# Kernel optimization log

Measured on AMD Instinct MI355X. Metric: run time of the kernel, lower is better.

Reference implementation:

```python
import jax, jax.numpy as jnp
import numpy as np

N, IN_DIM, HID, H1, NCLS, H2, E = 50000, 256, 32, 8, 16, 8, 800000


def gat_conv(x, edge_index, W, a_src, a_dst, b, H, C):
    """PyG-style GATConv, eval mode (attention dropout off), concat=True,
    negative_slope=0.2, add_self_loops=True."""
    n = x.shape[0]
    loop = jnp.arange(n)
    src = jnp.concatenate([edge_index[0], loop])  # [E+N]
    dst = jnp.concatenate([edge_index[1], loop])
    h = (x @ W).reshape(n, H, C)                  # [N,H,C]
    alpha_s = jnp.sum(h * a_src, axis=-1)         # [N,H]
    alpha_d = jnp.sum(h * a_dst, axis=-1)         # [N,H]
    e = jax.nn.leaky_relu(alpha_s[src] + alpha_d[dst], 0.2)  # [E+N,H]
    # segment softmax over incoming edges of each target node
    e_max = jax.ops.segment_max(e, dst, num_segments=n)      # [N,H] (self-loop guarantees nonempty)
    p = jnp.exp(e - e_max[dst])
    denom = jax.ops.segment_sum(p, dst, num_segments=n)
    alpha = p / (denom[dst] + 1e-16)              # [E+N,H]
    msg = h[src] * alpha[:, :, None]              # [E+N,H,C]
    out = jax.ops.segment_sum(msg, dst, num_segments=n)      # [N,H,C]
    return out.reshape(n, H * C) + b


def setup_inputs() -> dict:
    key = jax.random.key(0)
    ks = jax.random.split(key, 12)
    x = jax.random.normal(ks[0], (N, IN_DIM), dtype=jnp.float32)
    edge_index = jax.random.randint(ks[1], (2, E), 0, N, dtype=jnp.int64)
    s1 = 1.0 / np.sqrt(IN_DIM)
    s2 = 1.0 / np.sqrt(HID * H1)
    W1 = jax.random.normal(ks[2], (IN_DIM, H1 * HID), dtype=jnp.float32) * s1
    a_src1 = jax.random.normal(ks[3], (H1, HID), dtype=jnp.float32) * s1
    a_dst1 = jax.random.normal(ks[4], (H1, HID), dtype=jnp.float32) * s1
    b1 = jnp.zeros((H1 * HID,), dtype=jnp.float32)
    W2 = jax.random.normal(ks[5], (H1 * HID, H2 * NCLS), dtype=jnp.float32) * s2
    a_src2 = jax.random.normal(ks[6], (H2, NCLS), dtype=jnp.float32) * s2
    a_dst2 = jax.random.normal(ks[7], (H2, NCLS), dtype=jnp.float32) * s2
    b2 = jnp.zeros((H2 * NCLS,), dtype=jnp.float32)
    return {"x": x, "edge_index": edge_index, "W1": W1, "a_src1": a_src1,
            "a_dst1": a_dst1, "b1": b1, "W2": W2, "a_src2": a_src2,
            "a_dst2": a_dst2, "b2": b2}


def reference(x, edge_index, W1, a_src1, a_dst1, b1, W2, a_src2, a_dst2, b2):
    # eval mode: F.dropout is identity
    h = gat_conv(x, edge_index, W1, a_src1, a_dst1, b1, H1, HID)   # [N, H1*HID]
    h = jax.nn.elu(h)
    h = gat_conv(h, edge_index, W2, a_src2, a_dst2, b2, H2, NCLS)  # [N, H2*NCLS]
    return jax.nn.log_softmax(h, axis=1)
```

## Files before the change

### kernel.cpp

```cpp
#include <hip/hip_runtime.h>
#include <hip/hip_fp16.h>

#define NN 50000
#define NE 800000

typedef _Float16 half4v __attribute__((ext_vector_type(4)));
typedef _Float16 half8v __attribute__((ext_vector_type(8)));
typedef float f32x4 __attribute__((ext_vector_type(4)));

#define Q_SCALE 0.04724409448f
#define Q_INV   21.16666667f

static __device__ __forceinline__ float lrelu(float x) { return x > 0.f ? x : 0.2f * x; }

__global__ void detect_i64_kernel(const unsigned* __restrict__ ei, int* __restrict__ flag) {
  if (threadIdx.x == 0 && blockIdx.x == 0) {
    int is64 = 1;
    for (int i = 0; i < 64; ++i)
      if (ei[2 * i + 1] != 0u) { is64 = 0; break; }
    *flag = is64;
  }
}

static __device__ __forceinline__ int edge_at(const void* ei, int is64, long long idx) {
  if (is64) return (int)((const long long*)ei)[idx];
  return ((const int*)ei)[idx];
}

__global__ void count_kernel(const void* __restrict__ ei, const int* __restrict__ flag,
                             int* __restrict__ counts) {
  int e = blockIdx.x * blockDim.x + threadIdx.x;
  if (e >= NE) return;
  int is64 = *flag;
  int d = edge_at(ei, is64, (long long)NE + e);
  atomicAdd(&counts[d], 1);
}

static __device__ __forceinline__ int block_scan_inc(int v, int tid) {
  __shared__ int ws[4];
  const int lane = tid & 63, wv = tid >> 6;
  #pragma unroll
  for (int off = 1; off < 64; off <<= 1) {
    int t = __shfl_up(v, off);
    if (lane >= off) v += t;
  }
  if (lane == 63) ws[wv] = v;
  __syncthreads();
  int add = 0;
  #pragma unroll
  for (int j = 0; j < 4; ++j) if (j < wv) add += ws[j];
  return v + add;
}

__global__ void scan1_kernel(const int* __restrict__ counts, int* __restrict__ bsums) {
  __shared__ int ws[4];
  const int tid = threadIdx.x;
  const int lane = tid & 63, wv = tid >> 6;
  int i = blockIdx.x * 256 + tid;
  int v = (i < NN) ? counts[i] : 0;
  #pragma unroll
  for (int off = 1; off < 64; off <<= 1) v += __shfl_xor(v, off);
  if (lane == 0) ws[wv] = v;
  __syncthreads();
  if (tid == 0) bsums[blockIdx.x] = ws[0] + ws[1] + ws[2] + ws[3];
}

__global__ void scan2_kernel(int* __restrict__ bsums, int nb) {
  const int tid = threadIdx.x;
  int v = (tid < nb) ? bsums[tid] : 0;
  int inc = block_scan_inc(v, tid);
  if (tid < nb) bsums[tid] = inc - v;
}

__global__ void scan3_kernel(const int* __restrict__ counts, const int* __restrict__ bsums,
                             int* __restrict__ rs) {
  const int tid = threadIdx.x;
  int i = blockIdx.x * 256 + tid;
  int v = (i < NN) ? counts[i] : 0;
  int inc = block_scan_inc(v, tid);
  if (i < NN) rs[i + 1] = bsums[blockIdx.x] + inc;
  if (i == 0) rs[0] = 0;
}

__global__ void scatter_kernel(const void* __restrict__ ei, const int* __restrict__ flag,
                               const int* __restrict__ rs, int* __restrict__ cursor,
                               int* __restrict__ ssrc) {
  int e = blockIdx.x * blockDim.x + threadIdx.x;
  if (e >= NE) return;
  int is64 = *flag;
  int s = edge_at(ei, is64, e);
  int d = edge_at(ei, is64, (long long)NE + e);
  int p = atomicAdd(&cursor[d], 1);
  ssrc[rs[d] + p] = s;
}

__global__ void prep_kernel(const float* __restrict__ W1, const float* __restrict__ W2,
                            const float* __restrict__ aS1, const float* __restrict__ aD1,
                            const float* __restrict__ aS2, const float* __restrict__ aD2,
                            _Float16* __restrict__ W1p, _Float16* __restrict__ W2p,
                            _Float16* __restrict__ Wa1p, _Float16* __restrict__ Wa2p) {
  int i = blockIdx.x * blockDim.x + threadIdx.x;
  if (i < 65536) {
    int j = i & 7, l = (i >> 3) & 63, kst = (i >> 9) & 7, ct = i >> 12;
    int col = ct * 16 + (l & 15);
    int k = kst * 32 + ((l >> 4) << 3) + j;
    W1p[i] = (_Float16)W1[(size_t)k * 256 + col];
  } else if (i < 98304) {
    int n = i - 65536;
    int j = n & 7, l = (n >> 3) & 63, kst = (n >> 9) & 7, ct = n >> 12;
    int col = ct * 16 + (l & 15);
    int k = kst * 32 + ((l >> 4) << 3) + j;
    W2p[n] = (_Float16)W2[(size_t)k * 128 + col];
  } else if (i < 102400) {
    int n = i - 98304;
    int j = n & 7, l = (n >> 3) & 63, kst = n >> 9;
    int row = l & 15;
    int head = row & 7;
    const float* a = (row < 8) ? aS1 : aD1;
    int k = kst * 32 + ((l >> 4) << 3) + j;
    float s = 0.f;
    #pragma unroll 8
    for (int c = 0; c < 32; ++c)
      s += W1[(size_t)k * 256 + head * 32 + c] * a[head * 32 + c];
    Wa1p[n] = (_Float16)s;
  } else if (i < 106496) {
    int n = i - 102400;
    int j = n & 7, l = (n >> 3) & 63, kst = n >> 9;
    int row = l & 15;
    int head = row & 7;
    const float* a = (row < 8) ? aS2 : aD2;
    int k = kst * 32 + ((l >> 4) << 3) + j;
    float s = 0.f;
    #pragma unroll 8
    for (int c = 0; c < 16; ++c)
      s += W2[(size_t)k * 128 + head * 16 + c] * a[head * 16 + c];
    Wa2p[n] = (_Float16)s;
  }
}

template<int BN, int NCF, bool A_HALF, bool Q8OUT>
__global__ __launch_bounds__(512) void gemm_mfma(const void* __restrict__ Araw,
                                                 const _Float16* __restrict__ Bp,
                                                 const _Float16* __restrict__ Wap,
                                                 void* __restrict__ Cout,
                                                 float* __restrict__ alS,
                                                 float* __restrict__ alD, int M) {
  __shared__ __align__(16) _Float16 As[64][256 + 8];
  const int tid = threadIdx.x;
  const int bm0 = blockIdx.x * 64;
  if (A_HALF) {
    const _Float16* A = (const _Float16*)Araw;
    half8v tmp[4]; int rr[4], cc[4];
    #pragma unroll
    for (int t = 0; t < 4; ++t) {
      int idx = tid + t * 512;
      int r = idx >> 5, c8 = (idx & 31) << 3;
      int gr = bm0 + r;
      tmp[t] = (half8v){};
      if (gr < M) tmp[t] = *(const half8v*)&A[(size_t)gr * 256 + c8];
      rr[t] = r; cc[t] = c8;
    }
    #pragma unroll
    for (int t = 0; t < 4; ++t)
      *(half8v*)&As[rr[t]][cc[t]] = tmp[t];
  } else {
    const float* A = (const float*)Araw;
    #pragma unroll
    for (int g = 0; g < 2; ++g) {
      float4 tmp[4]; int rr[4], cc[4];
      #pragma unroll
      for (int t = 0; t < 4; ++t) {
        int idx = tid + (g * 4 + t) * 512;
        int r = idx >> 6, c4 = (idx & 63) << 2;
        int gr = bm0 + r;
        tmp[t] = make_float4(0.f, 0.f, 0.f, 0.f);
        if (gr < M) tmp[t] = *(const float4*)&A[(size_t)gr * 256 + c4];
        rr[t] = r; cc[t] = c4;
      }
      #pragma unroll
      for (int t = 0; t < 4; ++t) {
        half4v h = { (_Float16)tmp[t].x, (_Float16)tmp[t].y,
                     (_Float16)tmp[t].z, (_Float16)tmp[t].w };
        *(half4v*)&As[rr[t]][cc[t]] = h;
      }
    }
  }
  __syncthreads();
  const int lane = tid & 63, wv = tid >> 6;
  const int ncol0 = wv * (16 * NCF);
  const int lrow = lane & 15, lk8 = (lane >> 4) << 3;
  f32x4 acc[4][NCF];
  f32x4 acca[4];
  #pragma unroll
  for (int rf = 0; rf < 4; ++rf) {
    acca[rf] = (f32x4){0.f, 0.f, 0.f, 0.f};
    #pragma unroll
    for (int cf = 0; cf < NCF; ++cf) acc[rf][cf] = (f32x4){0.f, 0.f, 0.f, 0.f};
  }
  #pragma unroll
  for (int kst = 0; kst < 8; ++kst) {
    const int ks = kst * 32 + lk8;
    half8v af[4];
    #pragma unroll
    for (int rf = 0; rf < 4; ++rf)
      af[rf] = *(const half8v*)&As[16 * rf + lrow][ks];
    #pragma unroll
    for (int cf = 0; cf < NCF; ++cf) {
      half8v bf = *(const half8v*)&Bp[((size_t)((wv * NCF + cf) * 8 + kst) * 64 + lane) * 8];
      #pragma unroll
      for (int rf = 0; rf < 4; ++rf)
        acc[rf][cf] = __builtin_amdgcn_mfma_f32_16x16x32_f16(af[rf], bf, acc[rf][cf], 0, 0, 0);
    }
    if (wv == 0) {
      half8v bfa = *(const half8v*)&Wap[((size_t)kst * 64 + lane) * 8];
      #pragma unroll
      for (int rf = 0; rf < 4; ++rf)
        acca[rf] = __builtin_amdgcn_mfma_f32_16x16x32_f16(af[rf], bfa, acca[rf], 0, 0, 0);
    }
  }
  if (Q8OUT) {
    __syncthreads();
    constexpr int ROWB = BN + 16;
    char* Cs = (char*)&As[0][0];
    #pragma unroll
    for (int rf = 0; rf < 4; ++rf) {
      #pragma unroll
      for (int j = 0; j < 4; ++j) {
        int r = 16 * rf + 4 * ((lane >> 4) & 3) + j;
        #pragma unroll
        for (int cf = 0; cf < NCF; ++cf) {
          int col = ncol0 + 16 * cf + lrow;
          float v = acc[rf][cf][j];
          int q = __float2int_rn(fminf(fmaxf(v * Q_INV, -127.f), 127.f)) + 128;
          Cs[r * ROWB + col] = (char)q;
        }
      }
    }
    __syncthreads();
    unsigned char* C8 = (unsigned char*)Cout;
    for (int idx = tid; idx < 4 * BN; idx += 512) {
      int r = idx / (BN / 16), c16 = idx % (BN / 16);
      int grow = bm0 + r;
      if (grow < M)
        *(int4*)&C8[(size_t)grow * BN + 16 * c16] = *(const int4*)&Cs[r * ROWB + 16 * c16];
    }
  } else {
    __half* C = (__half*)Cout;
    #pragma unroll
    for (int rf = 0; rf < 4; ++rf) {
      #pragma unroll
      for (int j = 0; j < 4; ++j) {
        int row = bm0 + 16 * rf + 4 * ((lane >> 4) & 3) + j;
        if (row < M) {
          #pragma unroll
          for (int cf = 0; cf < NCF; ++cf) {
            int col = ncol0 + 16 * cf + lrow;
            C[(size_t)row * BN + col] = __float2half(acc[rf][cf][j]);
          }
        }
      }
    }
  }
  if (wv == 0) {
    #pragma unroll
    for (int rf = 0; rf < 4; ++rf) {
      #pragma unroll
      for (int j = 0; j < 4; ++j) {
        int row = bm0 + 16 * rf + 4 * ((lane >> 4) & 3) + j;
        if (row < M) {
          float v = acca[rf][j];
          if (lrow < 8) alS[row * 8 + lrow] = v;
          else          alD[row * 8 + (lrow - 8)] = v;
        }
      }
    }
  }
}

#define ACCQ(w, p) do { \
    ax0 += (p) * (float)((w) & 255u); \
    ax1 += (p) * (float)(((w) >> 8) & 255u); \
    ax2 += (p) * (float)(((w) >> 16) & 255u); \
    ax3 += (p) * (float)((w) >> 24); \
  } while (0)

__global__ __launch_bounds__(256) void agg1_kernel(const unsigned char* __restrict__ h1q,
    const float* __restrict__ as, const float* __restrict__ ad,
    const int* __restrict__ rs, const int* __restrict__ ssrc,
    const float* __restrict__ bias, __half* __restrict__ out) {
  const int wid = (blockIdx.x * blockDim.x + threadIdx.x) >> 6;
  const int lane = threadIdx.x & 63;
  if (wid >= NN) return;
  const int node = wid;
  const int beg = rs[node], end = rs[node + 1];
  const int deg = end - beg;
  const int hd = lane >> 3;
  const float advh = ad[node * 8 + hd];
  const unsigned* hw = (const unsigned*)h1q;
  float denom = 0.f;
  float ax0 = 0.f, ax1 = 0.f, ax2 = 0.f, ax3 = 0.f;
  {
    float p = __expf(lrelu(as[node * 8 + hd] + advh));
    unsigned w = hw[(size_t)node * 64 + lane];
    ACCQ(w, p);
    denom = p;
  }
  const int gb = lane & 56;
  for (int base = 0; base < deg; base += 64) {
    const int cnt = min(deg - base, 64);
    int sv = (lane < cnt) ? ssrc[beg + base + lane] : 0;
    int j = 0;
    for (; j + 8 <= cnt; j += 8) {
      int s0 = __builtin_amdgcn_readlane(sv, j + 0);
      int s1 = __builtin_amdgcn_readlane(sv, j + 1);
      int s2 = __builtin_amdgcn_readlane(sv, j + 2);
      int s3 = __builtin_amdgcn_readlane(sv, j + 3);
      int s4 = __builtin_amdgcn_readlane(sv, j + 4);
      int s5 = __builtin_amdgcn_readlane(sv, j + 5);
      int s6 = __builtin_amdgcn_readlane(sv, j + 6);
      int s7 = __builtin_amdgcn_readlane(sv, j + 7);
      unsigned w0 = hw[(size_t)s0 * 64 + lane];
      unsigned w1 = hw[(size_t)s1 * 64 + lane];
      unsigned w2 = hw[(size_t)s2 * 64 + lane];
      unsigned w3 = hw[(size_t)s3 * 64 + lane];
      unsigned w4 = hw[(size_t)s4 * 64 + lane];
      unsigned w5 = hw[(size_t)s5 * 64 + lane];
      unsigned w6 = hw[(size_t)s6 * 64 + lane];
      unsigned w7 = hw[(size_t)s7 * 64 + lane];
      int sl = __shfl(sv, j + (lane & 7));
      float pl = __expf(lrelu(as[(size_t)sl * 8 + hd] + advh));
      float p0 = __shfl(pl, gb + 0);
      float p1 = __shfl(pl, gb + 1);
      float p2 = __shfl(pl, gb + 2);
      float p3 = __shfl(pl, gb + 3);
      float p4 = __shfl(pl, gb + 4);
      float p5 = __shfl(pl, gb + 5);
      float p6 = __shfl(pl, gb + 6);
      float p7 = __shfl(pl, gb + 7);
      denom += (p0 + p1) + (p2 + p3) + ((p4 + p5) + (p6 + p7));
      ACCQ(w0, p0); ACCQ(w1, p1); ACCQ(w2, p2); ACCQ(w3, p3);
      ACCQ(w4, p4); ACCQ(w5, p5); ACCQ(w6, p6); ACCQ(w7, p7);
    }
    for (; j < cnt; ++j) {
      int s = __builtin_amdgcn_readlane(sv, j);
      float p = __expf(lrelu(as[s * 8 + hd] + advh));
      unsigned w = hw[(size_t)s * 64 + lane];
      ACCQ(w, p);
      denom += p;
    }
  }
  const float inv = 1.f / (denom + 1e-16f);
  const float4 bv = *(const float4*)&bias[lane * 4];
  float4 o;
  o.x = Q_SCALE * (ax0 * inv - 128.f) + bv.x;
  o.y = Q_SCALE * (ax1 * inv - 128.f) + bv.y;
  o.z = Q_SCALE * (ax2 * inv - 128.f) + bv.z;
  o.w = Q_SCALE * (ax3 * inv - 128.f) + bv.w;
  o.x = o.x > 0.f ? o.x : __expf(o.x) - 1.f;
  o.y = o.y > 0.f ? o.y : __expf(o.y) - 1.f;
  o.z = o.z > 0.f ? o.z : __expf(o.z) - 1.f;
  o.w = o.w > 0.f ? o.w : __expf(o.w) - 1.f;
  union { __half2 h2[2]; float2 f2; } w;
  w.h2[0] = __floats2half2_rn(o.x, o.y);
  w.h2[1] = __floats2half2_rn(o.z, o.w);
  *(float2*)&out[(size_t)node * 256 + lane * 4] = w.f2;
}

#define ACC2Q(w, p) do { \
    ax0 += (p) * (float)((w) & 255u); \
    ax1 += (p) * (float)(((w) >> 8) & 255u); \
  } while (0)

__global__ __launch_bounds__(256) void agg2_kernel(const unsigned char* __restrict__ h2q,
    const float* __restrict__ as, const float* __restrict__ ad,
    const int* __restrict__ rs, const int* __restrict__ ssrc,
    const float* __restrict__ bias, float* __restrict__ out) {
  const int wid = (blockIdx.x * blockDim.x + threadIdx.x) >> 6;
  const int lane = threadIdx.x & 63;
  if (wid >= NN) return;
  const int node = wid;
  const int beg = rs[node], end = rs[node + 1];
  const int deg = end - beg;
  const int hd = lane >> 3;
  const float advh = ad[node * 8 + hd];
  const unsigned short* hw = (const unsigned short*)h2q;
  float denom = 0.f;
  float ax0 = 0.f, ax1 = 0.f;
  {
    float p = __expf(lrelu(as[node * 8 + hd] + advh));
    unsigned w = hw[(size_t)node * 64 + lane];
    ACC2Q(w, p);
    denom = p;
  }
  const int gb = lane & 56;
  for (int base = 0; base < deg; base += 64) {
    const int cnt = min(deg - base, 64);
    int sv = (lane < cnt) ? ssrc[beg + base + lane] : 0;
    int j = 0;
    for (; j + 8 <= cnt; j += 8) {
      int s0 = __builtin_amdgcn_readlane(sv, j + 0);
      int s1 = __builtin_amdgcn_readlane(sv, j + 1);
      int s2 = __builtin_amdgcn_readlane(sv, j + 2);
      int s3 = __builtin_amdgcn_readlane(sv, j + 3);
      int s4 = __builtin_amdgcn_readlane(sv, j + 4);
      int s5 = __builtin_amdgcn_readlane(sv, j + 5);
      int s6 = __builtin_amdgcn_readlane(sv, j + 6);
      int s7 = __builtin_amdgcn_readlane(sv, j + 7);
      unsigned w0 = hw[(size_t)s0 * 64 + lane];
      unsigned w1 = hw[(size_t)s1 * 64 + lane];
      unsigned w2 = hw[(size_t)s2 * 64 + lane];
      unsigned w3 = hw[(size_t)s3 * 64 + lane];
      unsigned w4 = hw[(size_t)s4 * 64 + lane];
      unsigned w5 = hw[(size_t)s5 * 64 + lane];
      unsigned w6 = hw[(size_t)s6 * 64 + lane];
      unsigned w7 = hw[(size_t)s7 * 64 + lane];
      int sl = __shfl(sv, j + (lane & 7));
      float pl = __expf(lrelu(as[(size_t)sl * 8 + hd] + advh));
      float p0 = __shfl(pl, gb + 0);
      float p1 = __shfl(pl, gb + 1);
      float p2 = __shfl(pl, gb + 2);
      float p3 = __shfl(pl, gb + 3);
      float p4 = __shfl(pl, gb + 4);
      float p5 = __shfl(pl, gb + 5);
      float p6 = __shfl(pl, gb + 6);
      float p7 = __shfl(pl, gb + 7);
      denom += (p0 + p1) + (p2 + p3) + ((p4 + p5) + (p6 + p7));
      ACC2Q(w0, p0); ACC2Q(w1, p1); ACC2Q(w2, p2); ACC2Q(w3, p3);
      ACC2Q(w4, p4); ACC2Q(w5, p5); ACC2Q(w6, p6); ACC2Q(w7, p7);
    }
    for (; j < cnt; ++j) {
      int s = __builtin_amdgcn_readlane(sv, j);
      float p = __expf(lrelu(as[s * 8 + hd] + advh));
      unsigned w = hw[(size_t)s * 64 + lane];
      ACC2Q(w, p);
      denom += p;
    }
  }
  const float inv = 1.f / (denom + 1e-16f);
  float v0 = Q_SCALE * (ax0 * inv - 128.f) + bias[lane * 2 + 0];
  float v1 = Q_SCALE * (ax1 * inv - 128.f) + bias[lane * 2 + 1];
  float mx = fmaxf(v0, v1);
  #pragma unroll
  for (int off = 1; off < 64; off <<= 1) mx = fmaxf(mx, __shfl_xor(mx, off));
  float sum = __expf(v0 - mx) + __expf(v1 - mx);
  #pragma unroll
  for (int off = 1; off < 64; off <<= 1) sum += __shfl_xor(sum, off);
  float lse = mx + __logf(sum);
  float2 o = make_float2(v0 - lse, v1 - lse);
  __builtin_nontemporal_store(o.x, &out[(size_t)node * 128 + lane * 2]);
  __builtin_nontemporal_store(o.y, &out[(size_t)node * 128 + lane * 2 + 1]);
}

extern "C" void kernel_launch(void* const* d_in, const int* in_sizes, int n_in,
                              void* d_out, int out_size, void* d_ws, size_t ws_size,
                              hipStream_t stream) {
  const float* x    = (const float*)d_in[0];
  const void*  ei   = d_in[1];
  const float* W1   = (const float*)d_in[2];
  const float* aS1  = (const float*)d_in[3];
  const float* aD1  = (const float*)d_in[4];
  const float* b1   = (const float*)d_in[5];
  const float* W2   = (const float*)d_in[6];
  const float* aS2  = (const float*)d_in[7];
  const float* aD2  = (const float*)d_in[8];
  const float* b2   = (const float*)d_in[9];
  float* out = (float*)d_out;

  char* ws = (char*)d_ws;
  unsigned char* h1q = (unsigned char*)ws; ws += (size_t)NN * 256;
  unsigned char* h2q = (unsigned char*)ws; ws += (size_t)NN * 128;
  __half* hmid = (__half*)ws;          ws += (size_t)NN * 256 * 2;
  _Float16* W1p = (_Float16*)ws;       ws += (size_t)65536 * 2;
  _Float16* W2p = (_Float16*)ws;       ws += (size_t)32768 * 2;
  _Float16* Wa1p = (_Float16*)ws;      ws += (size_t)4096 * 2;
  _Float16* Wa2p = (_Float16*)ws;      ws += (size_t)4096 * 2;
  float* alS  = (float*)ws;            ws += (size_t)NN * 8 * 4;
  float* alD  = (float*)ws;            ws += (size_t)NN * 8 * 4;
  int* counts = (int*)ws;              ws += (size_t)NN * 4;
  int* rs     = (int*)ws;              ws += (size_t)(NN + 1) * 4;
  int* bsums  = (int*)ws;              ws += (size_t)256 * 4;
  int* ssrc   = (int*)ws;              ws += (size_t)NE * 4;
  int* flag   = (int*)ws;              ws += 256;

  const int NB = (NN + 255) / 256;

  detect_i64_kernel<<<1, 64, 0, stream>>>((const unsigned*)ei, flag);
  hipMemsetAsync(counts, 0, (size_t)NN * 4, stream);
  count_kernel<<<(NE + 255) / 256, 256, 0, stream>>>(ei, flag, counts);
  scan1_kernel<<<NB, 256, 0, stream>>>(counts, bsums);
  scan2_kernel<<<1, 256, 0, stream>>>(bsums, NB);
  scan3_kernel<<<NB, 256, 0, stream>>>(counts, bsums, rs);
  hipMemsetAsync(counts, 0, (size_t)NN * 4, stream);
  scatter_kernel<<<(NE + 255) / 256, 256, 0, stream>>>(ei, flag, rs, counts, ssrc);

  prep_kernel<<<(106496 + 255) / 256, 256, 0, stream>>>(W1, W2, aS1, aD1, aS2, aD2,
                                                        W1p, W2p, Wa1p, Wa2p);

  const int ngrid = (NN + 63) / 64;
  gemm_mfma<256, 2, false, true><<<ngrid, 512, 0, stream>>>(x, W1p, Wa1p, h1q, alS, alD, NN);
  agg1_kernel<<<(NN + 3) / 4, 256, 0, stream>>>(h1q, alS, alD, rs, ssrc, b1, hmid);

  gemm_mfma<128, 1, true, true><<<ngrid, 512, 0, stream>>>(hmid, W2p, Wa2p, h2q, alS, alD, NN);
  agg2_kernel<<<(NN + 3) / 4, 256, 0, stream>>>(h2q, alS, alD, rs, ssrc, b2, out);
}
```

Measured before the change: 222.8 us.

## Quantize hidden activations to int8, fuse count with weight prep, drop detect kernel

```diff
diff --git a/kernel.cpp b/kernel.cpp
--- a/kernel.cpp
+++ b/kernel.cpp
@@ -11,15 +11,16 @@
 #define Q_SCALE 0.04724409448f
 #define Q_INV   21.16666667f
 
+#define CVTB0(f, w) asm("v_cvt_f32_ubyte0 %0, %1" : "=v"(f) : "v"(w))
+#define CVTB1(f, w) asm("v_cvt_f32_ubyte1 %0, %1" : "=v"(f) : "v"(w))
+#define CVTB2(f, w) asm("v_cvt_f32_ubyte2 %0, %1" : "=v"(f) : "v"(w))
+#define CVTB3(f, w) asm("v_cvt_f32_ubyte3 %0, %1" : "=v"(f) : "v"(w))
+
 static __device__ __forceinline__ float lrelu(float x) { return x > 0.f ? x : 0.2f * x; }
 
-__global__ void detect_i64_kernel(const unsigned* __restrict__ ei, int* __restrict__ flag) {
-  if (threadIdx.x == 0 && blockIdx.x == 0) {
-    int is64 = 1;
-    for (int i = 0; i < 64; ++i)
-      if (ei[2 * i + 1] != 0u) { is64 = 0; break; }
-    *flag = is64;
-  }
+static __device__ __forceinline__ int detect64(const void* ei) {
+  const unsigned* w = (const unsigned*)ei;
+  return (w[1] | w[3] | w[5] | w[7]) == 0u;
 }
 
 static __device__ __forceinline__ int edge_at(const void* ei, int is64, long long idx) {
@@ -27,79 +28,20 @@
   return ((const int*)ei)[idx];
 }
 
-__global__ void count_kernel(const void* __restrict__ ei, const int* __restrict__ flag,
-                             int* __restrict__ counts) {
-  int e = blockIdx.x * blockDim.x + threadIdx.x;
-  if (e >= NE) return;
-  int is64 = *flag;
-  int d = edge_at(ei, is64, (long long)NE + e);
-  atomicAdd(&counts[d], 1);
-}
-
-static __device__ __forceinline__ int block_scan_inc(int v, int tid) {
-  __shared__ int ws[4];
-  const int lane = tid & 63, wv = tid >> 6;
-  #pragma unroll
-  for (int off = 1; off < 64; off <<= 1) {
-    int t = __shfl_up(v, off);
-    if (lane >= off) v += t;
-  }
-  if (lane == 63) ws[wv] = v;
-  __syncthreads();
-  int add = 0;
-  #pragma unroll
-  for (int j = 0; j < 4; ++j) if (j < wv) add += ws[j];
-  return v + add;
-}
-
-__global__ void scan1_kernel(const int* __restrict__ counts, int* __restrict__ bsums) {
-  __shared__ int ws[4];
-  const int tid = threadIdx.x;
-  const int lane = tid & 63, wv = tid >> 6;
-  int i = blockIdx.x * 256 + tid;
-  int v = (i < NN) ? counts[i] : 0;
-  #pragma unroll
-  for (int off = 1; off < 64; off <<= 1) v += __shfl_xor(v, off);
-  if (lane == 0) ws[wv] = v;
-  __syncthreads();
-  if (tid == 0) bsums[blockIdx.x] = ws[0] + ws[1] + ws[2] + ws[3];
-}
-
-__global__ void scan2_kernel(int* __restrict__ bsums, int nb) {
-  const int tid = threadIdx.x;
-  int v = (tid < nb) ? bsums[tid] : 0;
-  int inc = block_scan_inc(v, tid);
-  if (tid < nb) bsums[tid] = inc - v;
-}
-
-__global__ void scan3_kernel(const int* __restrict__ counts, const int* __restrict__ bsums,
-                             int* __restrict__ rs) {
-  const int tid = threadIdx.x;
-  int i = blockIdx.x * 256 + tid;
-  int v = (i < NN) ? counts[i] : 0;
-  int inc = block_scan_inc(v, tid);
-  if (i < NN) rs[i + 1] = bsums[blockIdx.x] + inc;
-  if (i == 0) rs[0] = 0;
-}
-
-__global__ void scatter_kernel(const void* __restrict__ ei, const int* __restrict__ flag,
-                               const int* __restrict__ rs, int* __restrict__ cursor,
-                               int* __restrict__ ssrc) {
-  int e = blockIdx.x * blockDim.x + threadIdx.x;
-  if (e >= NE) return;
-  int is64 = *flag;
-  int s = edge_at(ei, is64, e);
-  int d = edge_at(ei, is64, (long long)NE + e);
-  int p = atomicAdd(&cursor[d], 1);
-  ssrc[rs[d] + p] = s;
-}
-
-__global__ void prep_kernel(const float* __restrict__ W1, const float* __restrict__ W2,
-                            const float* __restrict__ aS1, const float* __restrict__ aD1,
-                            const float* __restrict__ aS2, const float* __restrict__ aD2,
-                            _Float16* __restrict__ W1p, _Float16* __restrict__ W2p,
-                            _Float16* __restrict__ Wa1p, _Float16* __restrict__ Wa2p) {
-  int i = blockIdx.x * blockDim.x + threadIdx.x;
+__global__ void count_prep_kernel(const void* __restrict__ ei, int* __restrict__ counts,
+                                  const float* __restrict__ W1, const float* __restrict__ W2,
+                                  const float* __restrict__ aS1, const float* __restrict__ aD1,
+                                  const float* __restrict__ aS2, const float* __restrict__ aD2,
+                                  _Float16* __restrict__ W1p, _Float16* __restrict__ W2p,
+                                  _Float16* __restrict__ Wa1p, _Float16* __restrict__ Wa2p) {
+  long long gid = (long long)blockIdx.x * blockDim.x + threadIdx.x;
+  if (gid < NE) {
+    int is64 = detect64(ei);
+    int d = edge_at(ei, is64, (long long)NE + gid);
+    atomicAdd(&counts[d], 1);
+    return;
+  }
+  int i = (int)(gid - NE);
   if (i < 65536) {
     int j = i & 7, l = (i >> 3) & 63, kst = (i >> 9) & 7, ct = i >> 12;
     int col = ct * 16 + (l & 15);
@@ -138,7 +80,65 @@
   }
 }
 
-template<int BN, int NCF, bool A_HALF, bool Q8OUT>
+static __device__ __forceinline__ int block_scan_inc(int v, int tid) {
+  __shared__ int ws[4];
+  const int lane = tid & 63, wv = tid >> 6;
+  #pragma unroll
+  for (int off = 1; off < 64; off <<= 1) {
+    int t = __shfl_up(v, off);
+    if (lane >= off) v += t;
+  }
+  if (lane == 63) ws[wv] = v;
+  __syncthreads();
+  int add = 0;
+  #pragma unroll
+  for (int j = 0; j < 4; ++j) if (j < wv) add += ws[j];
+  return v + add;
+}
+
+__global__ void scan1_kernel(const int* __restrict__ counts, int* __restrict__ bsums) {
+  __shared__ int ws[4];
+  const int tid = threadIdx.x;
+  const int lane = tid & 63, wv = tid >> 6;
+  int i = blockIdx.x * 256 + tid;
+  int v = (i < NN) ? counts[i] : 0;
+  #pragma unroll
+  for (int off = 1; off < 64; off <<= 1) v += __shfl_xor(v, off);
+  if (lane == 0) ws[wv] = v;
+  __syncthreads();
+  if (tid == 0) bsums[blockIdx.x] = ws[0] + ws[1] + ws[2] + ws[3];
+}
+
+__global__ void scan2_kernel(int* __restrict__ bsums, int nb) {
+  const int tid = threadIdx.x;
+  int v = (tid < nb) ? bsums[tid] : 0;
+  int inc = block_scan_inc(v, tid);
+  if (tid < nb) bsums[tid] = inc - v;
+}
+
+__global__ void scan3_kernel(const int* __restrict__ counts, const int* __restrict__ bsums,
+                             int* __restrict__ rs) {
+  const int tid = threadIdx.x;
+  int i = blockIdx.x * 256 + tid;
+  int v = (i < NN) ? counts[i] : 0;
+  int inc = block_scan_inc(v, tid);
+  if (i < NN) rs[i + 1] = bsums[blockIdx.x] + inc;
+  if (i == 0) rs[0] = 0;
+}
+
+__global__ void scatter_kernel(const void* __restrict__ ei,
+                               const int* __restrict__ rs, int* __restrict__ cursor,
+                               int* __restrict__ ssrc) {
+  int e = blockIdx.x * blockDim.x + threadIdx.x;
+  if (e >= NE) return;
+  int is64 = detect64(ei);
+  int s = edge_at(ei, is64, e);
+  int d = edge_at(ei, is64, (long long)NE + e);
+  int p = atomicAdd(&cursor[d], 1);
+  ssrc[rs[d] + p] = s;
+}
+
+template<int BN, int NCF, bool A_Q8, bool Q8OUT>
 __global__ __launch_bounds__(512) void gemm_mfma(const void* __restrict__ Araw,
                                                  const _Float16* __restrict__ Bp,
                                                  const _Float16* __restrict__ Wap,
@@ -148,21 +148,29 @@
   __shared__ __align__(16) _Float16 As[64][256 + 8];
   const int tid = threadIdx.x;
   const int bm0 = blockIdx.x * 64;
-  if (A_HALF) {
-    const _Float16* A = (const _Float16*)Araw;
-    half8v tmp[4]; int rr[4], cc[4];
-    #pragma unroll
-    for (int t = 0; t < 4; ++t) {
+  if (A_Q8) {
+    const unsigned char* A8 = (const unsigned char*)Araw;
+    #pragma unroll
+    for (int t = 0; t < 2; ++t) {
       int idx = tid + t * 512;
-      int r = idx >> 5, c8 = (idx & 31) << 3;
+      int r = idx >> 4, c16 = (idx & 15) << 4;
       int gr = bm0 + r;
-      tmp[t] = (half8v){};
-      if (gr < M) tmp[t] = *(const half8v*)&A[(size_t)gr * 256 + c8];
-      rr[t] = r; cc[t] = c8;
-    }
-    #pragma unroll
-    for (int t = 0; t < 4; ++t)
-      *(half8v*)&As[rr[t]][cc[t]] = tmp[t];
+      uint4 v = make_uint4(0x80808080u, 0x80808080u, 0x80808080u, 0x80808080u);
+      if (gr < M) v = *(const uint4*)&A8[(size_t)gr * 256 + c16];
+      unsigned dw[4] = { v.x, v.y, v.z, v.w };
+      _Float16 hb[16];
+      #pragma unroll
+      for (int d = 0; d < 4; ++d) {
+        float f0, f1, f2, f3;
+        CVTB0(f0, dw[d]); CVTB1(f1, dw[d]); CVTB2(f2, dw[d]); CVTB3(f3, dw[d]);
+        hb[4 * d + 0] = (_Float16)((f0 - 128.f) * Q_SCALE);
+        hb[4 * d + 1] = (_Float16)((f1 - 128.f) * Q_SCALE);
+        hb[4 * d + 2] = (_Float16)((f2 - 128.f) * Q_SCALE);
+        hb[4 * d + 3] = (_Float16)((f3 - 128.f) * Q_SCALE);
+      }
+      *(half8v*)&As[r][c16] = *(half8v*)&hb[0];
+      *(half8v*)&As[r][c16 + 8] = *(half8v*)&hb[8];
+    }
   } else {
     const float* A = (const float*)Araw;
     #pragma unroll
@@ -244,22 +252,6 @@
       if (grow < M)
         *(int4*)&C8[(size_t)grow * BN + 16 * c16] = *(const int4*)&Cs[r * ROWB + 16 * c16];
     }
-  } else {
-    __half* C = (__half*)Cout;
-    #pragma unroll
-    for (int rf = 0; rf < 4; ++rf) {
-      #pragma unroll
-      for (int j = 0; j < 4; ++j) {
-        int row = bm0 + 16 * rf + 4 * ((lane >> 4) & 3) + j;
-        if (row < M) {
-          #pragma unroll
-          for (int cf = 0; cf < NCF; ++cf) {
-            int col = ncol0 + 16 * cf + lrow;
-            C[(size_t)row * BN + col] = __float2half(acc[rf][cf][j]);
-          }
-        }
-      }
-    }
   }
   if (wv == 0) {
     #pragma unroll
@@ -278,16 +270,15 @@
 }
 
 #define ACCQ(w, p) do { \
-    ax0 += (p) * (float)((w) & 255u); \
-    ax1 += (p) * (float)(((w) >> 8) & 255u); \
-    ax2 += (p) * (float)(((w) >> 16) & 255u); \
-    ax3 += (p) * (float)((w) >> 24); \
+    float f0_, f1_, f2_, f3_; \
+    CVTB0(f0_, (w)); CVTB1(f1_, (w)); CVTB2(f2_, (w)); CVTB3(f3_, (w)); \
+    ax0 += (p) * f0_; ax1 += (p) * f1_; ax2 += (p) * f2_; ax3 += (p) * f3_; \
   } while (0)
 
 __global__ __launch_bounds__(256) void agg1_kernel(const unsigned char* __restrict__ h1q,
     const float* __restrict__ as, const float* __restrict__ ad,
     const int* __restrict__ rs, const int* __restrict__ ssrc,
-    const float* __restrict__ bias, __half* __restrict__ out) {
+    const float* __restrict__ bias, unsigned char* __restrict__ outq) {
   const int wid = (blockIdx.x * blockDim.x + threadIdx.x) >> 6;
   const int lane = threadIdx.x & 63;
   if (wid >= NN) return;
@@ -360,15 +351,18 @@
   o.y = o.y > 0.f ? o.y : __expf(o.y) - 1.f;
   o.z = o.z > 0.f ? o.z : __expf(o.z) - 1.f;
   o.w = o.w > 0.f ? o.w : __expf(o.w) - 1.f;
-  union { __half2 h2[2]; float2 f2; } w;
-  w.h2[0] = __floats2half2_rn(o.x, o.y);
-  w.h2[1] = __floats2half2_rn(o.z, o.w);
-  *(float2*)&out[(size_t)node * 256 + lane * 4] = w.f2;
+  int q0 = __float2int_rn(fminf(fmaxf(o.x * Q_INV, -127.f), 127.f)) + 128;
+  int q1 = __float2int_rn(fminf(fmaxf(o.y * Q_INV, -127.f), 127.f)) + 128;
+  int q2 = __float2int_rn(fminf(fmaxf(o.z * Q_INV, -127.f), 127.f)) + 128;
+  int q3 = __float2int_rn(fminf(fmaxf(o.w * Q_INV, -127.f), 127.f)) + 128;
+  unsigned pk = (unsigned)q0 | ((unsigned)q1 << 8) | ((unsigned)q2 << 16) | ((unsigned)q3 << 24);
+  ((unsigned*)outq)[(size_t)node * 64 + lane] = pk;
 }
 
 #define ACC2Q(w, p) do { \
-    ax0 += (p) * (float)((w) & 255u); \
-    ax1 += (p) * (float)(((w) >> 8) & 255u); \
+    float f0_, f1_; \
+    CVTB0(f0_, (w)); CVTB1(f1_, (w)); \
+    ax0 += (p) * f0_; ax1 += (p) * f1_; \
   } while (0)
 
 __global__ __launch_bounds__(256) void agg2_kernel(const unsigned char* __restrict__ h2q,
@@ -468,8 +462,8 @@
 
   char* ws = (char*)d_ws;
   unsigned char* h1q = (unsigned char*)ws; ws += (size_t)NN * 256;
+  unsigned char* hmq = (unsigned char*)ws; ws += (size_t)NN * 256;
   unsigned char* h2q = (unsigned char*)ws; ws += (size_t)NN * 128;
-  __half* hmid = (__half*)ws;          ws += (size_t)NN * 256 * 2;
   _Float16* W1p = (_Float16*)ws;       ws += (size_t)65536 * 2;
   _Float16* W2p = (_Float16*)ws;       ws += (size_t)32768 * 2;
   _Float16* Wa1p = (_Float16*)ws;      ws += (size_t)4096 * 2;
@@ -477,29 +471,28 @@
   float* alS  = (float*)ws;            ws += (size_t)NN * 8 * 4;
   float* alD  = (float*)ws;            ws += (size_t)NN * 8 * 4;
   int* counts = (int*)ws;              ws += (size_t)NN * 4;
+  int* cursor = (int*)ws;              ws += (size_t)NN * 4;
   int* rs     = (int*)ws;              ws += (size_t)(NN + 1) * 4;
   int* bsums  = (int*)ws;              ws += (size_t)256 * 4;
   int* ssrc   = (int*)ws;              ws += (size_t)NE * 4;
-  int* flag   = (int*)ws;              ws += 256;
 
   const int NB = (NN + 255) / 256;
 
-  detect_i64_kernel<<<1, 64, 0, stream>>>((const unsigned*)ei, flag);
-  hipMemsetAsync(counts, 0, (size_t)NN * 4, stream);
-  count_kernel<<<(NE + 255) / 256, 256, 0, stream>>>(ei, flag, counts);
+  hipMemsetAsync(counts, 0, (size_t)2 * NN * 4, stream);
+
+  const long long total_cp = (long long)NE + 106496;
+  count_prep_kernel<<<(int)((total_cp + 255) / 256), 256, 0, stream>>>(
+      ei, counts, W1, W2, aS1, aD1, aS2, aD2, W1p, W2p, Wa1p, Wa2p);
+
   scan1_kernel<<<NB, 256, 0, stream>>>(counts, bsums);
   scan2_kernel<<<1, 256, 0, stream>>>(bsums, NB);
   scan3_kernel<<<NB, 256, 0, stream>>>(counts, bsums, rs);
-  hipMemsetAsync(counts, 0, (size_t)NN * 4, stream);
-  scatter_kernel<<<(NE + 255) / 256, 256, 0, stream>>>(ei, flag, rs, counts, ssrc);
-
-  prep_kernel<<<(106496 + 255) / 256, 256, 0, stream>>>(W1, W2, aS1, aD1, aS2, aD2,
-                                                        W1p, W2p, Wa1p, Wa2p);
+  scatter_kernel<<<(NE + 255) / 256, 256, 0, stream>>>(ei, rs, cursor, ssrc);
 
   const int ngrid = (NN + 63) / 64;
   gemm_mfma<256, 2, false, true><<<ngrid, 512, 0, stream>>>(x, W1p, Wa1p, h1q, alS, alD, NN);
-  agg1_kernel<<<(NN + 3) / 4, 256, 0, stream>>>(h1q, alS, alD, rs, ssrc, b1, hmid);
-
-  gemm_mfma<128, 1, true, true><<<ngrid, 512, 0, stream>>>(hmid, W2p, Wa2p, h2q, alS, alD, NN);
+  agg1_kernel<<<(NN + 3) / 4, 256, 0, stream>>>(h1q, alS, alD, rs, ssrc, b1, hmq);
+
+  gemm_mfma<128, 1, true, true><<<ngrid, 512, 0, stream>>>(hmq, W2p, Wa2p, h2q, alS, alD, NN);
   agg2_kernel<<<(NN + 3) / 4, 256, 0, stream>>>(h2q, alS, alD, rs, ssrc, b2, out);
 }
```

Result: faster. 215.6 us (-3.2%).
